# Performance work log

Measured on AMD Instinct MI355X. Metric: run time of the kernel, lower is better.

Reference implementation:

```python
import jax, jax.numpy as jnp
import numpy as np
from jax import lax

C = 8          # bargs.channel
S = 1024       # bargs.test_sidelen
SIGMA = 1.0    # edge_sigma
KS = int(6 * SIGMA + 1)   # 7
PAD = KS // 2             # 3
BW = S // 6               # border_width
LAM, MU, TH = 5.0, 5.0, 1e-4


def _edge_kernel():
    coords = jnp.arange(KS, dtype=jnp.float32) - (KS - 1.0) / 2.0
    g1 = jnp.exp(-coords ** 2 / (2.0 * SIGMA ** 2))
    g1 = g1 / g1.sum()
    g2 = jnp.outer(g1, g1)
    return jnp.broadcast_to(g2, (C, 1, KS, KS))  # depthwise OIHW


def _alpha():
    # max applicable loop index among {row-dist, col-dist}; interior stays 1.
    r = jnp.arange(S)
    g = jnp.where(r < BW, r, jnp.where(S - 1 - r < BW, S - 1 - r, -1))  # [S]
    m = jnp.maximum(g[:, None], g[None, :])                              # [S,S]
    a = jnp.where(m >= 0, m.astype(jnp.float32) / BW, 1.0)
    return a[None, None]  # [1,1,S,S] broadcasts over channels


def _grad_spectrum():
    gv = jnp.array([[-1., -2., -1.], [0., 0., 0.], [1., 2., 1.]], jnp.float32)
    gh = gv.T
    gvf = jnp.fft.fft2(gv, s=(S, S))
    ghf = jnp.fft.fft2(gh, s=(S, S))
    return (jnp.abs(gvf) ** 2 + jnp.abs(ghf) ** 2).astype(jnp.float32)  # real


def _edge_blur(img, kernel, alpha):
    blurred = lax.conv_general_dilated(
        img, kernel, window_strides=(1, 1), padding=[(PAD, PAD), (PAD, PAD)],
        feature_group_count=C, dimension_numbers=('NCHW', 'OIHW', 'NCHW'))
    return alpha * img + (1.0 - alpha) * blurred


def setup_inputs() -> dict:
    key = jax.random.key(0)
    k1, k2 = jax.random.split(key)
    lms = jax.random.uniform(k1, (1, C, S, S), dtype=jnp.float32)
    fuse = jax.random.uniform(k2, (1, C, S, S), dtype=jnp.float32)
    return {"lms": lms, "fuse": fuse}


def reference(lms, fuse):
    kernel = _edge_kernel()
    alpha = _alpha()
    grad = _grad_spectrum()

    lms_fft = jnp.fft.fft2(_edge_blur(lms, kernel, alpha))
    fuse_fft = jnp.fft.fft2(_edge_blur(fuse, kernel, alpha))

    denom = jnp.abs(fuse_fft) ** 2 + LAM + MU * grad      # real [1,C,S,S]
    numer = jnp.conj(fuse_fft) * lms_fft
    psf = jnp.fft.fftshift(jnp.real(jnp.fft.ifft2(numer / denom)), axes=(-2, -1))
    psf = jnp.where(psf < TH, 0.0, psf)                   # [1,C,S,S]

    def crop(p):  # p: [S,S]
        row, col = jnp.unravel_index(jnp.argmax(p), p.shape)
        patch = lax.dynamic_slice(p, (row - 20, col - 20), (41, 41))
        return patch / jnp.sum(patch)

    psf_l = jax.vmap(crop)(psf[0])        # [C,41,41]
    return psf_l[:, None]                 # [C,1,41,41]
```

## Files before the change

### kernel.cpp

```cpp
#include <hip/hip_runtime.h>
#include <math.h>

#define SS 1024
#define NC 8
#define BWD 170
#define THRESH 1e-4f

typedef unsigned long long ull;

__device__ __forceinline__ float2 cmul(float2 a, float2 b) {
    return make_float2(a.x * b.x - a.y * b.y, a.x * b.y + a.y * b.x);
}

#define XS(a) ((a) ^ (((a) >> 4) & 15))

template <int DIR>
__device__ __forceinline__ void bfly4(const float2 v[4], float2 r[4]) {
    float2 a = v[0], b = v[1], c = v[2], d = v[3];
    float2 apc = make_float2(a.x + c.x, a.y + c.y);
    float2 amc = make_float2(a.x - c.x, a.y - c.y);
    float2 bpd = make_float2(b.x + d.x, b.y + d.y);
    float2 jb  = make_float2(-(b.y - d.y), b.x - d.x);
    r[0] = make_float2(apc.x + bpd.x, apc.y + bpd.y);
    r[2] = make_float2(apc.x - bpd.x, apc.y - bpd.y);
    if (DIR == -1) {
        r[1] = make_float2(amc.x - jb.x, amc.y - jb.y);
        r[3] = make_float2(amc.x + jb.x, amc.y + jb.y);
    } else {
        r[1] = make_float2(amc.x + jb.x, amc.y + jb.y);
        r[3] = make_float2(amc.x - jb.x, amc.y - jb.y);
    }
}

template <int DIR>
__device__ __forceinline__ void fft1024_reg(float2 v[4], float2* A, float2* B,
                                            int tid) {
    float2* dst = A;
    float2* alt = B;
    #pragma unroll
    for (int t = 0; t < 4; ++t) {
        int s = 1 << (2 * t);
        int k = tid & ~(s - 1);
        float2 r[4];
        bfly4<DIR>(v, r);
        float rev = (float)k * (1.0f / 1024.0f);
        float2 w1 = make_float2(__builtin_amdgcn_cosf(rev),
                                (float)DIR * __builtin_amdgcn_sinf(rev));
        float2 w2 = cmul(w1, w1);
        float2 w3 = cmul(w2, w1);
        int base = tid + 3 * k;
        dst[XS(base)]         = r[0];
        dst[XS(base + s)]     = cmul(r[1], w1);
        dst[XS(base + 2 * s)] = cmul(r[2], w2);
        dst[XS(base + 3 * s)] = cmul(r[3], w3);
        __syncthreads();
        v[0] = dst[XS(tid)];
        v[1] = dst[XS(tid + 256)];
        v[2] = dst[XS(tid + 512)];
        v[3] = dst[XS(tid + 768)];
        float2* tmp = dst; dst = alt; alt = tmp;
    }
    float2 r[4];
    bfly4<DIR>(v, r);
    v[0] = r[0]; v[1] = r[1]; v[2] = r[2]; v[3] = r[3];
}

#define PIDX(r) ((r) + ((r) >> 5))

__global__ __launch_bounds__(256) void blur_fft_kernel(
        const float* __restrict__ lms, const float* __restrict__ fuse,
        float2* __restrict__ Zf) {
    __shared__ float2 bufA[1024];
    __shared__ float2 smemB2[1068];
    float* rowl = (float*)smemB2;
    float* rowf = rowl + 1068;
    int tid = threadIdx.x;
    int g = blockIdx.x;
    int c = g >> 10;
    int y = (g & 7) * 128 + ((g >> 3) & 127);
    const float* L = lms + ((size_t)c << 20);
    const float* F = fuse + ((size_t)c << 20);
    int x0 = tid << 2;

    double e1 = exp(-0.5), e2 = exp(-2.0), e3 = exp(-4.5);
    double sm = 1.0 + 2.0 * (e1 + e2 + e3);
    float w[7] = { (float)(e3 / sm), (float)(e2 / sm), (float)(e1 / sm),
                   (float)(1.0 / sm),
                   (float)(e1 / sm), (float)(e2 / sm), (float)(e3 / sm) };

    bool rowInt = (y >= BWD) && (y <= SS - 1 - BWD);
    bool skipLoads = rowInt && (tid >= 45) && (tid <= 210);
    bool doH = !rowInt || (tid <= 43) || (tid >= 212);

    float4 cl, cf;
    if (skipLoads) {
        cl = *(const float4*)&L[((size_t)y << 10) + x0];
        cf = *(const float4*)&F[((size_t)y << 10) + x0];
    } else {
        float4 lv[7], fv[7];
        #pragma unroll
        for (int r = 0; r < 7; ++r) {
            int gy = y - 3 + r;
            if (gy >= 0 && gy < SS) {
                lv[r] = *(const float4*)&L[((size_t)gy << 10) + x0];
                fv[r] = *(const float4*)&F[((size_t)gy << 10) + x0];
            } else {
                lv[r] = make_float4(0.f, 0.f, 0.f, 0.f);
                fv[r] = make_float4(0.f, 0.f, 0.f, 0.f);
            }
        }
        cl = lv[3]; cf = fv[3];
        #pragma unroll
        for (int j = 0; j < 4; ++j) {
            float a = 0.f, b = 0.f;
            #pragma unroll
            for (int r = 0; r < 7; ++r) {
                a += w[r] * (&lv[r].x)[j];
                b += w[r] * (&fv[r].x)[j];
            }
            rowl[PIDX(3 + x0 + j)] = a;
            rowf[PIDX(3 + x0 + j)] = b;
        }
    }
    if (tid < 3) {
        rowl[PIDX(tid)] = 0.f; rowf[PIDX(tid)] = 0.f;
        rowl[PIDX(1027 + tid)] = 0.f; rowf[PIDX(1027 + tid)] = 0.f;
    }
    __syncthreads();

    float bl[4] = {0.f, 0.f, 0.f, 0.f}, bf[4] = {0.f, 0.f, 0.f, 0.f};
    if (doH) {
        #pragma unroll
        for (int k = 0; k < 4; ++k) {
            float a = 0.f, b = 0.f;
            #pragma unroll
            for (int j = 0; j < 7; ++j) {
                a += w[j] * rowl[PIDX(x0 + k + j)];
                b += w[j] * rowf[PIDX(x0 + k + j)];
            }
            bl[k] = a; bf[k] = b;
        }
    }
    int gyv = (y < BWD) ? y : ((SS - 1 - y) < BWD ? (SS - 1 - y) : -1);
    #pragma unroll
    for (int k = 0; k < 4; ++k) {
        int x = x0 + k;
        int gx = (x < BWD) ? x : ((SS - 1 - x) < BWD ? (SS - 1 - x) : -1);
        int m = gyv > gx ? gyv : gx;
        float a = (m >= 0) ? (float)m / (float)BWD : 1.0f;
        bufA[XS(x)] = make_float2(a * (&cl.x)[k] + (1.0f - a) * bl[k],
                                  a * (&cf.x)[k] + (1.0f - a) * bf[k]);
    }
    __syncthreads();

    float2 v[4];
    #pragma unroll
    for (int m = 0; m < 4; ++m) v[m] = bufA[XS(tid + (m << 8))];
    fft1024_reg<-1>(v, smemB2, bufA, tid);

    float2* Zrow = Zf + (((size_t)c << 20) + ((size_t)y << 10));
    #pragma unroll
    for (int r = 0; r < 4; ++r) Zrow[tid + (r << 8)] = v[r];
}

__global__ __launch_bounds__(256) void fft2_wiener_kernel(
        const float2* __restrict__ Z, float2* __restrict__ Wb) {
    __shared__ float2 resbuf[4][1024];
    __shared__ float2 scratch[1024];
    int tid = threadIdx.x;
    int p = blockIdx.x >> 9;
    int i = blockIdx.x & 511;
    int rows[2];
    rows[0] = (i == 0) ? 0 : i;
    rows[1] = (i == 0) ? 512 : 1024 - i;
    bool selfp = (i == 0);

    float2 v[4], nv[4];
    {
        const float2* g0 = Z + (((size_t)(2 * p) << 20) +
                                ((size_t)rows[0] << 10));
        #pragma unroll
        for (int m = 0; m < 4; ++m) v[m] = g0[tid + (m << 8)];
    }
    #pragma unroll
    for (int combo = 0; combo < 4; ++combo) {
        if (combo < 3) {
            int nr = (combo + 1) >> 1, nc = (combo + 1) & 1;
            const float2* gn = Z + (((size_t)(2 * p + nc) << 20) +
                                    ((size_t)rows[nr] << 10));
            #pragma unroll
            for (int m = 0; m < 4; ++m) nv[m] = gn[tid + (m << 8)];
        }
        fft1024_reg<-1>(v, scratch, resbuf[combo], tid);
        #pragma unroll
        for (int r = 0; r < 4; ++r)
            resbuf[combo][XS(tid + (r << 8))] = v[r];
        if (combo < 3) {
            #pragma unroll
            for (int m = 0; m < 4; ++m) v[m] = nv[m];
        }
    }
    __syncthreads();

    float2 gout[2][4];
    #pragma unroll
    for (int o = 0; o < 2; ++o) {
        int u = rows[o];
        int po = selfp ? o : (1 - o);
        float cu = __builtin_amdgcn_cosf((float)u * (1.0f / 1024.0f));
        float c2u = 2.0f * cu * cu - 1.0f;
        float hu = 2.0f + 2.0f * cu;
        #pragma unroll
        for (int j = 0; j < 4; ++j) {
            int vv = tid + (j << 8);
            int vn = (1024 - vv) & 1023;
            float cv = __builtin_amdgcn_cosf((float)vv * (1.0f / 1024.0f));
            float c2v = 2.0f * cv * cv - 1.0f;
            float hv = 2.0f + 2.0f * cv;
            float grad = (2.0f - 2.0f * c2v) * hu * hu +
                         (2.0f - 2.0f * c2u) * hv * hv;
            float regs = 5.0f + 5.0f * grad;
            float G0x, G0y, G1x, G1y;
            #pragma unroll
            for (int c = 0; c < 2; ++c) {
                float2 a = resbuf[o * 2 + c][XS(vv)];
                float2 b = resbuf[po * 2 + c][XS(vn)];
                float Lx = 0.5f * (a.x + b.x), Ly = 0.5f * (a.y - b.y);
                float Fx = 0.5f * (a.y + b.y), Fy = -0.5f * (a.x - b.x);
                float inv = 1.0f / (Fx * Fx + Fy * Fy + regs);
                float nx = (Fx * Lx + Fy * Ly) * inv;
                float ny = (Fx * Ly - Fy * Lx) * inv;
                if (c == 0) { G0x = nx; G0y = ny; } else { G1x = nx; G1y = ny; }
            }
            gout[o][j] = make_float2(G0x - G1y, G0y + G1x);
        }
    }
    __syncthreads();

    const float isc = 1.0f / 1024.0f;
    #pragma unroll
    for (int o = 0; o < 2; ++o) {
        float2 iv[4];
        #pragma unroll
        for (int j = 0; j < 4; ++j) iv[j] = gout[o][j];
        fft1024_reg<1>(iv, scratch, resbuf[o], tid);
        float2* go = Wb + (((size_t)p << 20) + ((size_t)rows[o] << 10));
        #pragma unroll
        for (int r = 0; r < 4; ++r)
            go[tid + (r << 8)] = make_float2(iv[r].x * isc, iv[r].y * isc);
    }
}

__global__ __launch_bounds__(256) void ifft_final_kernel(
        const float2* __restrict__ Wd, float* __restrict__ psf,
        ull* __restrict__ bm) {
    __shared__ float2 bufA[1024];
    __shared__ float2 bufB[1024];
    __shared__ ull red0[4];
    __shared__ ull red1[4];
    int tid = threadIdx.x;
    const float2* g = Wd + ((size_t)blockIdx.x << 10);
    float2 v[4];
    #pragma unroll
    for (int m = 0; m < 4; ++m) v[m] = g[tid + (m << 8)];
    fft1024_reg<1>(v, bufA, bufB, tid);

    int p = blockIdx.x >> 10;
    int y = blockIdx.x & 1023;
    int oy = (y + 512) & 1023;
    float* p0 = psf + (((size_t)(2 * p) << 20) + ((size_t)oy << 10));
    float* p1 = p0 + (1u << 20);
    const float sc = 1.0f / 1024.0f;
    ull e0 = 0, e1 = 0;
    #pragma unroll
    for (int r = 0; r < 4; ++r) {
        int k = tid + (r << 8);
        float re = v[r].x * sc; re = (re < THRESH) ? 0.0f : re;
        float im = v[r].y * sc; im = (im < THRESH) ? 0.0f : im;
        int ox = (k + 512) & 1023;
        p0[ox] = re;
        p1[ox] = im;
        unsigned int idx = ((unsigned int)oy << 10) | (unsigned int)ox;
        ull c0 = ((ull)__float_as_uint(re) << 32) | (ull)(0xFFFFFFFFu - idx);
        ull c1 = ((ull)__float_as_uint(im) << 32) | (ull)(0xFFFFFFFFu - idx);
        e0 = c0 > e0 ? c0 : e0;
        e1 = c1 > e1 ? c1 : e1;
    }
    #pragma unroll
    for (int off = 32; off > 0; off >>= 1) {
        ull o0 = __shfl_down(e0, off);
        ull o1 = __shfl_down(e1, off);
        e0 = o0 > e0 ? o0 : e0;
        e1 = o1 > e1 ? o1 : e1;
    }
    if ((tid & 63) == 0) { red0[tid >> 6] = e0; red1[tid >> 6] = e1; }
    __syncthreads();
    if (tid == 0) {
        ull m0 = red0[0], m1 = red1[0];
        #pragma unroll
        for (int i2 = 1; i2 < 4; ++i2) {
            m0 = red0[i2] > m0 ? red0[i2] : m0;
            m1 = red1[i2] > m1 ? red1[i2] : m1;
        }
        bm[((size_t)(2 * p) << 10) + y] = m0;
        bm[((size_t)(2 * p + 1) << 10) + y] = m1;
    }
}

__global__ __launch_bounds__(256) void transpose_kernel(float2* __restrict__ A) {
    __shared__ float2 ta[32][33];
    __shared__ float2 tb[32][33];
    float2* P = A + ((size_t)blockIdx.y << 20);
    int r = blockIdx.x, bi = 0;
    while (r >= 32 - bi) { r -= 32 - bi; ++bi; }
    int bj = bi + r;
    int tx = threadIdx.x & 15;
    int ty = threadIdx.x >> 4;
    #pragma unroll
    for (int yy0 = 0; yy0 < 32; yy0 += 16) {
        int yy = yy0 + ty;
        float4 va = *(const float4*)&P[(size_t)(bi * 32 + yy) * SS + bj * 32 + 2 * tx];
        float4 vb = *(const float4*)&P[(size_t)(bj * 32 + yy) * SS + bi * 32 + 2 * tx];
        ta[yy][2 * tx]     = make_float2(va.x, va.y);
        ta[yy][2 * tx + 1] = make_float2(va.z, va.w);
        tb[yy][2 * tx]     = make_float2(vb.x, vb.y);
        tb[yy][2 * tx + 1] = make_float2(vb.z, vb.w);
    }
    __syncthreads();
    #pragma unroll
    for (int yy0 = 0; yy0 < 32; yy0 += 16) {
        int yy = yy0 + ty;
        float2 a0 = tb[2 * tx][yy], a1 = tb[2 * tx + 1][yy];
        *(float4*)&P[(size_t)(bi * 32 + yy) * SS + bj * 32 + 2 * tx] =
            make_float4(a0.x, a0.y, a1.x, a1.y);
        float2 b0 = ta[2 * tx][yy], b1 = ta[2 * tx + 1][yy];
        *(float4*)&P[(size_t)(bj * 32 + yy) * SS + bi * 32 + 2 * tx] =
            make_float4(b0.x, b0.y, b1.x, b1.y);
    }
}

__global__ __launch_bounds__(256) void crop_kernel(
        const float* __restrict__ psf, const ull* __restrict__ bm,
        float* __restrict__ out) {
    int c = blockIdx.x;
    __shared__ ull rmax[256];
    __shared__ float red[256];
    int tid = threadIdx.x;
    ull e = 0;
    for (int i = tid; i < 1024; i += 256) {
        ull v = bm[((size_t)c << 10) + i];
        e = v > e ? v : e;
    }
    rmax[tid] = e;
    __syncthreads();
    for (int s2 = 128; s2 > 0; s2 >>= 1) {
        if (tid < s2) { ull a = rmax[tid], b = rmax[tid + s2]; rmax[tid] = a > b ? a : b; }
        __syncthreads();
    }
    unsigned int bidx = 0xFFFFFFFFu - (unsigned int)(rmax[0] & 0xFFFFFFFFull);
    int row = (int)(bidx >> 10), col = (int)(bidx & 1023);
    int r0 = row - 20; if (r0 < 0) r0 = 0; if (r0 > SS - 41) r0 = SS - 41;
    int c0 = col - 20; if (c0 < 0) c0 = 0; if (c0 > SS - 41) c0 = SS - 41;
    const float* p = psf + ((size_t)c << 20);
    float local = 0.0f;
    for (int i = tid; i < 1681; i += 256) {
        int rr = i / 41, cc = i - rr * 41;
        local += p[(size_t)(r0 + rr) * SS + c0 + cc];
    }
    red[tid] = local;
    __syncthreads();
    for (int s2 = 128; s2 > 0; s2 >>= 1) {
        if (tid < s2) red[tid] += red[tid + s2];
        __syncthreads();
    }
    float inv = 1.0f / red[0];
    for (int i = tid; i < 1681; i += 256) {
        int rr = i / 41, cc = i - rr * 41;
        out[c * 1681 + i] = p[(size_t)(r0 + rr) * SS + c0 + cc] * inv;
    }
}

extern "C" void kernel_launch(void* const* d_in, const int* in_sizes, int n_in,
                              void* d_out, int out_size, void* d_ws,
                              size_t ws_size, hipStream_t stream) {
    const float* lms = (const float*)d_in[0];
    const float* fuse = (const float*)d_in[1];
    char* ws = (char*)d_ws;
    float2* Zf = (float2*)ws;
    float2* Wb = (float2*)(ws + ((size_t)64 << 20));
    float* psf = (float*)ws;
    ull* bm = (ull*)(ws + ((size_t)33 << 20));
    float* outp = (float*)d_out;

    blur_fft_kernel<<<8192, 256, 0, stream>>>(lms, fuse, Zf);
    transpose_kernel<<<dim3(528, 8), 256, 0, stream>>>(Zf);
    fft2_wiener_kernel<<<2048, 256, 0, stream>>>(Zf, Wb);
    transpose_kernel<<<dim3(528, 4), 256, 0, stream>>>(Wb);
    ifft_final_kernel<<<4096, 256, 0, stream>>>(Wb, psf, bm);
    crop_kernel<<<8, 256, 0, stream>>>(psf, bm, outp);
}
```

Measured before the change: 210.1 us.

## Compute each 1024-point FFT within a single wavefront using radix-16 stages

```diff
diff --git a/kernel.cpp b/kernel.cpp
--- a/kernel.cpp
+++ b/kernel.cpp
@@ -33,54 +33,109 @@
 }
 
 template <int DIR>
-__device__ __forceinline__ void fft1024_reg(float2 v[4], float2* A, float2* B,
-                                            int tid) {
-    float2* dst = A;
-    float2* alt = B;
-    #pragma unroll
-    for (int t = 0; t < 4; ++t) {
-        int s = 1 << (2 * t);
-        int k = tid & ~(s - 1);
+__device__ __forceinline__ float2 wc(float2 a, float cr, float si) {
+    float s = (DIR == -1) ? -si : si;
+    return make_float2(a.x * cr - a.y * s, a.x * s + a.y * cr);
+}
+
+template <int DIR>
+__device__ __forceinline__ void dft16_tw(float2 u[16], float rev) {
+    float2 t[4][4];
+    #pragma unroll
+    for (int a = 0; a < 4; ++a) {
+        float2 in[4] = { u[a], u[a + 4], u[a + 8], u[a + 12] };
+        bfly4<DIR>(in, t[a]);
+    }
+    const float C1 = 0.923879532511287f, S1 = 0.382683432365090f;
+    const float C2 = 0.707106781186548f;
+    t[1][1] = wc<DIR>(t[1][1], C1, S1);
+    t[1][2] = wc<DIR>(t[1][2], C2, C2);
+    t[1][3] = wc<DIR>(t[1][3], S1, C1);
+    t[2][1] = wc<DIR>(t[2][1], C2, C2);
+    t[2][2] = (DIR == -1) ? make_float2(t[2][2].y, -t[2][2].x)
+                          : make_float2(-t[2][2].y, t[2][2].x);
+    t[2][3] = wc<DIR>(t[2][3], -C2, C2);
+    t[3][1] = wc<DIR>(t[3][1], S1, C1);
+    t[3][2] = wc<DIR>(t[3][2], -C2, C2);
+    t[3][3] = wc<DIR>(t[3][3], -C1, -S1);
+    #pragma unroll
+    for (int ci = 0; ci < 4; ++ci) {
+        float2 in[4] = { t[0][ci], t[1][ci], t[2][ci], t[3][ci] };
+        float2 s[4];
+        bfly4<DIR>(in, s);
+        u[ci] = s[0]; u[ci + 4] = s[1]; u[ci + 8] = s[2]; u[ci + 12] = s[3];
+    }
+    float cs = __builtin_amdgcn_cosf(rev);
+    float sn = __builtin_amdgcn_sinf(rev);
+    float2 w1 = make_float2(cs, (float)DIR * sn);
+    float2 w2 = cmul(w1, w1);
+    float2 w3 = cmul(w2, w1);
+    float2 w4 = cmul(w2, w2);
+    float2 w8 = cmul(w4, w4);
+    u[1]  = cmul(u[1], w1);
+    u[2]  = cmul(u[2], w2);
+    u[3]  = cmul(u[3], w3);
+    u[4]  = cmul(u[4], w4);
+    u[5]  = cmul(u[5], cmul(w4, w1));
+    u[6]  = cmul(u[6], cmul(w4, w2));
+    u[7]  = cmul(u[7], cmul(w4, w3));
+    u[8]  = cmul(u[8], w8);
+    u[9]  = cmul(u[9], cmul(w8, w1));
+    u[10] = cmul(u[10], cmul(w8, w2));
+    u[11] = cmul(u[11], cmul(w8, w3));
+    u[12] = cmul(u[12], cmul(w8, w4));
+    u[13] = cmul(u[13], cmul(w8, cmul(w4, w1)));
+    u[14] = cmul(u[14], cmul(w8, cmul(w4, w2)));
+    u[15] = cmul(u[15], cmul(w8, cmul(w4, w3)));
+}
+
+template <int DIR>
+__device__ __forceinline__ void fft1024_wave(float2 v[16], float2* X, int l) {
+    dft16_tw<DIR>(v, (float)l * (1.0f / 1024.0f));
+    int base = l << 4;
+    #pragma unroll
+    for (int cc = 0; cc < 16; ++cc) X[XS(base + cc)] = v[cc];
+    asm volatile("s_waitcnt lgkmcnt(0)" ::: "memory");
+    int a_ = l & 3, cr = l >> 2;
+    #pragma unroll
+    for (int b = 0; b < 16; ++b)
+        v[b] = X[XS(((a_ + (b << 2)) << 4) + cr)];
+    asm volatile("s_waitcnt lgkmcnt(0)" ::: "memory");
+    dft16_tw<DIR>(v, (float)a_ * (1.0f / 64.0f));
+    #pragma unroll
+    for (int cc = 0; cc < 16; ++cc) X[XS(base + cc)] = v[cc];
+    asm volatile("s_waitcnt lgkmcnt(0)" ::: "memory");
+    int c2 = l & 15, cl2 = l >> 4;
+    float2 q[16];
+    #pragma unroll
+    for (int a2 = 0; a2 < 4; ++a2)
+        #pragma unroll
+        for (int chh = 0; chh < 4; ++chh)
+            q[(a2 << 2) + chh] =
+                X[XS(((a2 + (c2 << 2)) << 4) + cl2 + (chh << 2))];
+    asm volatile("s_waitcnt lgkmcnt(0)" ::: "memory");
+    #pragma unroll
+    for (int chh = 0; chh < 4; ++chh) {
+        float2 in[4] = { q[chh], q[4 + chh], q[8 + chh], q[12 + chh] };
         float2 r[4];
-        bfly4<DIR>(v, r);
-        float rev = (float)k * (1.0f / 1024.0f);
-        float2 w1 = make_float2(__builtin_amdgcn_cosf(rev),
-                                (float)DIR * __builtin_amdgcn_sinf(rev));
-        float2 w2 = cmul(w1, w1);
-        float2 w3 = cmul(w2, w1);
-        int base = tid + 3 * k;
-        dst[XS(base)]         = r[0];
-        dst[XS(base + s)]     = cmul(r[1], w1);
-        dst[XS(base + 2 * s)] = cmul(r[2], w2);
-        dst[XS(base + 3 * s)] = cmul(r[3], w3);
-        __syncthreads();
-        v[0] = dst[XS(tid)];
-        v[1] = dst[XS(tid + 256)];
-        v[2] = dst[XS(tid + 512)];
-        v[3] = dst[XS(tid + 768)];
-        float2* tmp = dst; dst = alt; alt = tmp;
-    }
-    float2 r[4];
-    bfly4<DIR>(v, r);
-    v[0] = r[0]; v[1] = r[1]; v[2] = r[2]; v[3] = r[3];
-}
-
-#define PIDX(r) ((r) + ((r) >> 5))
+        bfly4<DIR>(in, r);
+        v[chh] = r[0]; v[chh + 4] = r[1]; v[chh + 8] = r[2]; v[chh + 12] = r[3];
+    }
+}
 
 __global__ __launch_bounds__(256) void blur_fft_kernel(
         const float* __restrict__ lms, const float* __restrict__ fuse,
         float2* __restrict__ Zf) {
-    __shared__ float2 bufA[1024];
-    __shared__ float2 smemB2[1068];
-    float* rowl = (float*)smemB2;
-    float* rowf = rowl + 1068;
+    __shared__ float2 xch[4][1024];
     int tid = threadIdx.x;
+    int wv = tid >> 6, l = tid & 63;
     int g = blockIdx.x;
-    int c = g >> 10;
-    int y = (g & 7) * 128 + ((g >> 3) & 127);
+    int c = g >> 8;
+    int rg = (g & 7) * 32 + ((g >> 3) & 31);
+    int y = (rg << 2) + wv;
     const float* L = lms + ((size_t)c << 20);
     const float* F = fuse + ((size_t)c << 20);
-    int x0 = tid << 2;
+    float2* X = xch[wv];
 
     double e1 = exp(-0.5), e2 = exp(-2.0), e3 = exp(-4.5);
     double sm = 1.0 + 2.0 * (e1 + e2 + e3);
@@ -89,130 +144,107 @@
                    (float)(e1 / sm), (float)(e2 / sm), (float)(e3 / sm) };
 
     bool rowInt = (y >= BWD) && (y <= SS - 1 - BWD);
-    bool skipLoads = rowInt && (tid >= 45) && (tid <= 210);
-    bool doH = !rowInt || (tid <= 43) || (tid >= 212);
-
-    float4 cl, cf;
-    if (skipLoads) {
-        cl = *(const float4*)&L[((size_t)y << 10) + x0];
-        cf = *(const float4*)&F[((size_t)y << 10) + x0];
+    bool skipB = rowInt && (l >= 11) && (l <= 52);
+    int gyv = (y < BWD) ? y : ((SS - 1 - y) < BWD ? (SS - 1 - y) : -1);
+
+    if (skipB) {
+        #pragma unroll
+        for (int m = 0; m < 4; ++m) {
+            float4 cl = *(const float4*)&L[((size_t)y << 10) + (l << 4) + (m << 2)];
+            float4 cf = *(const float4*)&F[((size_t)y << 10) + (l << 4) + (m << 2)];
+            #pragma unroll
+            for (int n = 0; n < 4; ++n)
+                X[XS((l << 4) + (m << 2) + n)] =
+                    make_float2((&cl.x)[n], (&cf.x)[n]);
+        }
     } else {
-        float4 lv[7], fv[7];
+        float accL[24], accF[24];
+        #pragma unroll
+        for (int j = 0; j < 24; ++j) { accL[j] = 0.f; accF[j] = 0.f; }
         #pragma unroll
         for (int r = 0; r < 7; ++r) {
             int gy = y - 3 + r;
-            if (gy >= 0 && gy < SS) {
-                lv[r] = *(const float4*)&L[((size_t)gy << 10) + x0];
-                fv[r] = *(const float4*)&F[((size_t)gy << 10) + x0];
-            } else {
-                lv[r] = make_float4(0.f, 0.f, 0.f, 0.f);
-                fv[r] = make_float4(0.f, 0.f, 0.f, 0.f);
+            if (gy < 0 || gy >= SS) continue;
+            const float* Lr = L + ((size_t)gy << 10);
+            const float* Fr = F + ((size_t)gy << 10);
+            float wr = w[r];
+            #pragma unroll
+            for (int q = 0; q < 6; ++q) {
+                int f = (l << 2) - 1 + q;
+                if (f >= 0 && f < 256) {
+                    float4 vl = *(const float4*)&Lr[f << 2];
+                    float4 vf = *(const float4*)&Fr[f << 2];
+                    accL[(q << 2) + 0] += wr * vl.x; accF[(q << 2) + 0] += wr * vf.x;
+                    accL[(q << 2) + 1] += wr * vl.y; accF[(q << 2) + 1] += wr * vf.y;
+                    accL[(q << 2) + 2] += wr * vl.z; accF[(q << 2) + 2] += wr * vf.z;
+                    accL[(q << 2) + 3] += wr * vl.w; accF[(q << 2) + 3] += wr * vf.w;
+                }
             }
         }
-        cl = lv[3]; cf = fv[3];
-        #pragma unroll
-        for (int j = 0; j < 4; ++j) {
-            float a = 0.f, b = 0.f;
+        #pragma unroll
+        for (int m = 0; m < 4; ++m) {
+            float4 cl = *(const float4*)&L[((size_t)y << 10) + (l << 4) + (m << 2)];
+            float4 cf = *(const float4*)&F[((size_t)y << 10) + (l << 4) + (m << 2)];
             #pragma unroll
-            for (int r = 0; r < 7; ++r) {
-                a += w[r] * (&lv[r].x)[j];
-                b += w[r] * (&fv[r].x)[j];
+            for (int n = 0; n < 4; ++n) {
+                int k = (m << 2) + n;
+                float bl = 0.f, bf = 0.f;
+                #pragma unroll
+                for (int j = 0; j < 7; ++j) {
+                    bl += w[j] * accL[k + 1 + j];
+                    bf += w[j] * accF[k + 1 + j];
+                }
+                int x = (l << 4) + k;
+                int gx = (x < BWD) ? x : ((SS - 1 - x) < BWD ? (SS - 1 - x) : -1);
+                int mm = gyv > gx ? gyv : gx;
+                float a = (mm >= 0) ? (float)mm * (1.0f / BWD) : 1.0f;
+                X[XS((l << 4) + k)] = make_float2(
+                    a * (&cl.x)[n] + (1.0f - a) * bl,
+                    a * (&cf.x)[n] + (1.0f - a) * bf);
             }
-            rowl[PIDX(3 + x0 + j)] = a;
-            rowf[PIDX(3 + x0 + j)] = b;
         }
     }
-    if (tid < 3) {
-        rowl[PIDX(tid)] = 0.f; rowf[PIDX(tid)] = 0.f;
-        rowl[PIDX(1027 + tid)] = 0.f; rowf[PIDX(1027 + tid)] = 0.f;
-    }
-    __syncthreads();
-
-    float bl[4] = {0.f, 0.f, 0.f, 0.f}, bf[4] = {0.f, 0.f, 0.f, 0.f};
-    if (doH) {
-        #pragma unroll
-        for (int k = 0; k < 4; ++k) {
-            float a = 0.f, b = 0.f;
-            #pragma unroll
-            for (int j = 0; j < 7; ++j) {
-                a += w[j] * rowl[PIDX(x0 + k + j)];
-                b += w[j] * rowf[PIDX(x0 + k + j)];
-            }
-            bl[k] = a; bf[k] = b;
-        }
-    }
-    int gyv = (y < BWD) ? y : ((SS - 1 - y) < BWD ? (SS - 1 - y) : -1);
-    #pragma unroll
-    for (int k = 0; k < 4; ++k) {
-        int x = x0 + k;
-        int gx = (x < BWD) ? x : ((SS - 1 - x) < BWD ? (SS - 1 - x) : -1);
-        int m = gyv > gx ? gyv : gx;
-        float a = (m >= 0) ? (float)m / (float)BWD : 1.0f;
-        bufA[XS(x)] = make_float2(a * (&cl.x)[k] + (1.0f - a) * bl[k],
-                                  a * (&cf.x)[k] + (1.0f - a) * bf[k]);
-    }
-    __syncthreads();
-
-    float2 v[4];
-    #pragma unroll
-    for (int m = 0; m < 4; ++m) v[m] = bufA[XS(tid + (m << 8))];
-    fft1024_reg<-1>(v, smemB2, bufA, tid);
-
+    asm volatile("s_waitcnt lgkmcnt(0)" ::: "memory");
+    float2 v[16];
+    #pragma unroll
+    for (int b = 0; b < 16; ++b) v[b] = X[XS(l + (b << 6))];
+    fft1024_wave<-1>(v, X, l);
     float2* Zrow = Zf + (((size_t)c << 20) + ((size_t)y << 10));
     #pragma unroll
-    for (int r = 0; r < 4; ++r) Zrow[tid + (r << 8)] = v[r];
+    for (int j = 0; j < 16; ++j) Zrow[l + (j << 6)] = v[j];
 }
 
 __global__ __launch_bounds__(256) void fft2_wiener_kernel(
         const float2* __restrict__ Z, float2* __restrict__ Wb) {
-    __shared__ float2 resbuf[4][1024];
-    __shared__ float2 scratch[1024];
+    __shared__ float2 xch[4][1024];
     int tid = threadIdx.x;
+    int wv = tid >> 6, l = tid & 63;
     int p = blockIdx.x >> 9;
     int i = blockIdx.x & 511;
-    int rows[2];
-    rows[0] = (i == 0) ? 0 : i;
-    rows[1] = (i == 0) ? 512 : 1024 - i;
     bool selfp = (i == 0);
-
-    float2 v[4], nv[4];
-    {
-        const float2* g0 = Z + (((size_t)(2 * p) << 20) +
-                                ((size_t)rows[0] << 10));
-        #pragma unroll
-        for (int m = 0; m < 4; ++m) v[m] = g0[tid + (m << 8)];
-    }
-    #pragma unroll
-    for (int combo = 0; combo < 4; ++combo) {
-        if (combo < 3) {
-            int nr = (combo + 1) >> 1, nc = (combo + 1) & 1;
-            const float2* gn = Z + (((size_t)(2 * p + nc) << 20) +
-                                    ((size_t)rows[nr] << 10));
-            #pragma unroll
-            for (int m = 0; m < 4; ++m) nv[m] = gn[tid + (m << 8)];
-        }
-        fft1024_reg<-1>(v, scratch, resbuf[combo], tid);
-        #pragma unroll
-        for (int r = 0; r < 4; ++r)
-            resbuf[combo][XS(tid + (r << 8))] = v[r];
-        if (combo < 3) {
-            #pragma unroll
-            for (int m = 0; m < 4; ++m) v[m] = nv[m];
-        }
-    }
+    int row0 = selfp ? 0 : i;
+    int row1 = selfp ? 512 : 1024 - i;
+    int ch = wv & 1;
+    int myrow = (wv & 2) ? row1 : row0;
+    const float2* g0 = Z + (((size_t)(2 * p + ch) << 20) + ((size_t)myrow << 10));
+    float2 v[16];
+    #pragma unroll
+    for (int b = 0; b < 16; ++b) v[b] = g0[l + (b << 6)];
+    fft1024_wave<-1>(v, xch[wv], l);
+    #pragma unroll
+    for (int j = 0; j < 16; ++j) xch[wv][XS(l + (j << 6))] = v[j];
     __syncthreads();
 
-    float2 gout[2][4];
-    #pragma unroll
-    for (int o = 0; o < 2; ++o) {
-        int u = rows[o];
-        int po = selfp ? o : (1 - o);
+    float2 gi[16];
+    if (wv < 2) {
+        int u = wv ? row1 : row0;
+        int po = selfp ? wv : (1 - wv);
         float cu = __builtin_amdgcn_cosf((float)u * (1.0f / 1024.0f));
         float c2u = 2.0f * cu * cu - 1.0f;
         float hu = 2.0f + 2.0f * cu;
         #pragma unroll
-        for (int j = 0; j < 4; ++j) {
-            int vv = tid + (j << 8);
+        for (int j = 0; j < 16; ++j) {
+            int vv = l + (j << 6);
             int vn = (1024 - vv) & 1023;
             float cv = __builtin_amdgcn_cosf((float)vv * (1.0f / 1024.0f));
             float c2v = 2.0f * cv * cv - 1.0f;
@@ -222,61 +254,57 @@
             float regs = 5.0f + 5.0f * grad;
             float G0x, G0y, G1x, G1y;
             #pragma unroll
-            for (int c = 0; c < 2; ++c) {
-                float2 a = resbuf[o * 2 + c][XS(vv)];
-                float2 b = resbuf[po * 2 + c][XS(vn)];
+            for (int cc = 0; cc < 2; ++cc) {
+                float2 a = xch[wv * 2 + cc][XS(vv)];
+                float2 b = xch[po * 2 + cc][XS(vn)];
                 float Lx = 0.5f * (a.x + b.x), Ly = 0.5f * (a.y - b.y);
                 float Fx = 0.5f * (a.y + b.y), Fy = -0.5f * (a.x - b.x);
                 float inv = 1.0f / (Fx * Fx + Fy * Fy + regs);
                 float nx = (Fx * Lx + Fy * Ly) * inv;
                 float ny = (Fx * Ly - Fy * Lx) * inv;
-                if (c == 0) { G0x = nx; G0y = ny; } else { G1x = nx; G1y = ny; }
+                if (cc == 0) { G0x = nx; G0y = ny; } else { G1x = nx; G1y = ny; }
             }
-            gout[o][j] = make_float2(G0x - G1y, G0y + G1x);
+            gi[j] = make_float2(G0x - G1y, G0y + G1x);
         }
     }
     __syncthreads();
 
-    const float isc = 1.0f / 1024.0f;
-    #pragma unroll
-    for (int o = 0; o < 2; ++o) {
-        float2 iv[4];
-        #pragma unroll
-        for (int j = 0; j < 4; ++j) iv[j] = gout[o][j];
-        fft1024_reg<1>(iv, scratch, resbuf[o], tid);
-        float2* go = Wb + (((size_t)p << 20) + ((size_t)rows[o] << 10));
-        #pragma unroll
-        for (int r = 0; r < 4; ++r)
-            go[tid + (r << 8)] = make_float2(iv[r].x * isc, iv[r].y * isc);
+    if (wv < 2) {
+        fft1024_wave<1>(gi, xch[wv], l);
+        const float isc = 1.0f / 1024.0f;
+        int orow = wv ? row1 : row0;
+        float2* go = Wb + (((size_t)p << 20) + ((size_t)orow << 10));
+        #pragma unroll
+        for (int j = 0; j < 16; ++j)
+            go[l + (j << 6)] = make_float2(gi[j].x * isc, gi[j].y * isc);
     }
 }
 
 __global__ __launch_bounds__(256) void ifft_final_kernel(
         const float2* __restrict__ Wd, float* __restrict__ psf,
         ull* __restrict__ bm) {
-    __shared__ float2 bufA[1024];
-    __shared__ float2 bufB[1024];
-    __shared__ ull red0[4];
-    __shared__ ull red1[4];
+    __shared__ float2 xch[4][1024];
     int tid = threadIdx.x;
-    const float2* g = Wd + ((size_t)blockIdx.x << 10);
-    float2 v[4];
-    #pragma unroll
-    for (int m = 0; m < 4; ++m) v[m] = g[tid + (m << 8)];
-    fft1024_reg<1>(v, bufA, bufB, tid);
-
-    int p = blockIdx.x >> 10;
-    int y = blockIdx.x & 1023;
+    int wv = tid >> 6, l = tid & 63;
+    int R = blockIdx.x * 4 + wv;
+    const float2* g = Wd + ((size_t)R << 10);
+    float2 v[16];
+    #pragma unroll
+    for (int b = 0; b < 16; ++b) v[b] = g[l + (b << 6)];
+    fft1024_wave<1>(v, xch[wv], l);
+
+    int p = R >> 10;
+    int y = R & 1023;
     int oy = (y + 512) & 1023;
     float* p0 = psf + (((size_t)(2 * p) << 20) + ((size_t)oy << 10));
     float* p1 = p0 + (1u << 20);
     const float sc = 1.0f / 1024.0f;
     ull e0 = 0, e1 = 0;
     #pragma unroll
-    for (int r = 0; r < 4; ++r) {
-        int k = tid + (r << 8);
-        float re = v[r].x * sc; re = (re < THRESH) ? 0.0f : re;
-        float im = v[r].y * sc; im = (im < THRESH) ? 0.0f : im;
+    for (int j = 0; j < 16; ++j) {
+        int k = l + (j << 6);
+        float re = v[j].x * sc; re = (re < THRESH) ? 0.0f : re;
+        float im = v[j].y * sc; im = (im < THRESH) ? 0.0f : im;
         int ox = (k + 512) & 1023;
         p0[ox] = re;
         p1[ox] = im;
@@ -293,17 +321,9 @@
         e0 = o0 > e0 ? o0 : e0;
         e1 = o1 > e1 ? o1 : e1;
     }
-    if ((tid & 63) == 0) { red0[tid >> 6] = e0; red1[tid >> 6] = e1; }
-    __syncthreads();
-    if (tid == 0) {
-        ull m0 = red0[0], m1 = red1[0];
-        #pragma unroll
-        for (int i2 = 1; i2 < 4; ++i2) {
-            m0 = red0[i2] > m0 ? red0[i2] : m0;
-            m1 = red1[i2] > m1 ? red1[i2] : m1;
-        }
-        bm[((size_t)(2 * p) << 10) + y] = m0;
-        bm[((size_t)(2 * p + 1) << 10) + y] = m1;
+    if (l == 0) {
+        bm[((size_t)(2 * p) << 10) + y] = e0;
+        bm[((size_t)(2 * p + 1) << 10) + y] = e1;
     }
 }
 
@@ -392,10 +412,10 @@
     ull* bm = (ull*)(ws + ((size_t)33 << 20));
     float* outp = (float*)d_out;
 
-    blur_fft_kernel<<<8192, 256, 0, stream>>>(lms, fuse, Zf);
+    blur_fft_kernel<<<2048, 256, 0, stream>>>(lms, fuse, Zf);
     transpose_kernel<<<dim3(528, 8), 256, 0, stream>>>(Zf);
     fft2_wiener_kernel<<<2048, 256, 0, stream>>>(Zf, Wb);
     transpose_kernel<<<dim3(528, 4), 256, 0, stream>>>(Wb);
-    ifft_final_kernel<<<4096, 256, 0, stream>>>(Wb, psf, bm);
+    ifft_final_kernel<<<1024, 256, 0, stream>>>(Wb, psf, bm);
     crop_kernel<<<8, 256, 0, stream>>>(psf, bm, outp);
 }
```

Measured after the change: 240.3 us. 14.4% more time.

## Drop explicit transposes and read FFT columns with strided loads

Applied to the files above, without the earlier changes.

```diff
diff --git a/kernel.cpp b/kernel.cpp
--- a/kernel.cpp
+++ b/kernel.cpp
@@ -169,7 +169,8 @@
     __shared__ float2 scratch[1024];
     int tid = threadIdx.x;
     int p = blockIdx.x >> 9;
-    int i = blockIdx.x & 511;
+    int i0 = blockIdx.x & 511;
+    int i = ((i0 & 7) << 3) | ((i0 >> 3) & 7) | (i0 & ~63);
     int rows[2];
     rows[0] = (i == 0) ? 0 : i;
     rows[1] = (i == 0) ? 512 : 1024 - i;
@@ -177,19 +178,19 @@
 
     float2 v[4], nv[4];
     {
-        const float2* g0 = Z + (((size_t)(2 * p) << 20) +
-                                ((size_t)rows[0] << 10));
-        #pragma unroll
-        for (int m = 0; m < 4; ++m) v[m] = g0[tid + (m << 8)];
+        const float2* g0 = Z + (((size_t)(2 * p) << 20) + rows[0]);
+        #pragma unroll
+        for (int m = 0; m < 4; ++m)
+            v[m] = g0[(size_t)(tid + (m << 8)) << 10];
     }
     #pragma unroll
     for (int combo = 0; combo < 4; ++combo) {
         if (combo < 3) {
             int nr = (combo + 1) >> 1, nc = (combo + 1) & 1;
-            const float2* gn = Z + (((size_t)(2 * p + nc) << 20) +
-                                    ((size_t)rows[nr] << 10));
-            #pragma unroll
-            for (int m = 0; m < 4; ++m) nv[m] = gn[tid + (m << 8)];
+            const float2* gn = Z + (((size_t)(2 * p + nc) << 20) + rows[nr]);
+            #pragma unroll
+            for (int m = 0; m < 4; ++m)
+                nv[m] = gn[(size_t)(tid + (m << 8)) << 10];
         }
         fft1024_reg<-1>(v, scratch, resbuf[combo], tid);
         #pragma unroll
@@ -259,14 +260,16 @@
     __shared__ ull red0[4];
     __shared__ ull red1[4];
     int tid = threadIdx.x;
-    const float2* g = Wd + ((size_t)blockIdx.x << 10);
+    int p = blockIdx.x >> 10;
+    int b0 = blockIdx.x & 1023;
+    int y = ((b0 & 7) << 3) | ((b0 >> 3) & 7) | (b0 & ~63);
+    const float2* g = Wd + (((size_t)p << 20) + y);
     float2 v[4];
     #pragma unroll
-    for (int m = 0; m < 4; ++m) v[m] = g[tid + (m << 8)];
+    for (int m = 0; m < 4; ++m)
+        v[m] = g[(size_t)(tid + (m << 8)) << 10];
     fft1024_reg<1>(v, bufA, bufB, tid);
 
-    int p = blockIdx.x >> 10;
-    int y = blockIdx.x & 1023;
     int oy = (y + 512) & 1023;
     float* p0 = psf + (((size_t)(2 * p) << 20) + ((size_t)oy << 10));
     float* p1 = p0 + (1u << 20);
@@ -307,38 +310,6 @@
     }
 }
 
-__global__ __launch_bounds__(256) void transpose_kernel(float2* __restrict__ A) {
-    __shared__ float2 ta[32][33];
-    __shared__ float2 tb[32][33];
-    float2* P = A + ((size_t)blockIdx.y << 20);
-    int r = blockIdx.x, bi = 0;
-    while (r >= 32 - bi) { r -= 32 - bi; ++bi; }
-    int bj = bi + r;
-    int tx = threadIdx.x & 15;
-    int ty = threadIdx.x >> 4;
-    #pragma unroll
-    for (int yy0 = 0; yy0 < 32; yy0 += 16) {
-        int yy = yy0 + ty;
-        float4 va = *(const float4*)&P[(size_t)(bi * 32 + yy) * SS + bj * 32 + 2 * tx];
-        float4 vb = *(const float4*)&P[(size_t)(bj * 32 + yy) * SS + bi * 32 + 2 * tx];
-        ta[yy][2 * tx]     = make_float2(va.x, va.y);
-        ta[yy][2 * tx + 1] = make_float2(va.z, va.w);
-        tb[yy][2 * tx]     = make_float2(vb.x, vb.y);
-        tb[yy][2 * tx + 1] = make_float2(vb.z, vb.w);
-    }
-    __syncthreads();
-    #pragma unroll
-    for (int yy0 = 0; yy0 < 32; yy0 += 16) {
-        int yy = yy0 + ty;
-        float2 a0 = tb[2 * tx][yy], a1 = tb[2 * tx + 1][yy];
-        *(float4*)&P[(size_t)(bi * 32 + yy) * SS + bj * 32 + 2 * tx] =
-            make_float4(a0.x, a0.y, a1.x, a1.y);
-        float2 b0 = ta[2 * tx][yy], b1 = ta[2 * tx + 1][yy];
-        *(float4*)&P[(size_t)(bj * 32 + yy) * SS + bi * 32 + 2 * tx] =
-            make_float4(b0.x, b0.y, b1.x, b1.y);
-    }
-}
-
 __global__ __launch_bounds__(256) void crop_kernel(
         const float* __restrict__ psf, const ull* __restrict__ bm,
         float* __restrict__ out) {
@@ -393,9 +364,7 @@
     float* outp = (float*)d_out;
 
     blur_fft_kernel<<<8192, 256, 0, stream>>>(lms, fuse, Zf);
-    transpose_kernel<<<dim3(528, 8), 256, 0, stream>>>(Zf);
     fft2_wiener_kernel<<<2048, 256, 0, stream>>>(Zf, Wb);
-    transpose_kernel<<<dim3(528, 4), 256, 0, stream>>>(Wb);
     ifft_final_kernel<<<4096, 256, 0, stream>>>(Wb, psf, bm);
     crop_kernel<<<8, 256, 0, stream>>>(psf, bm, outp);
 }
```

Measured after the change: 207.7 us. Within noise of the previous version (-1.1%).
